# Kernel tuning notes

Hardware: AMD Instinct MI355X
Metric: run time of the kernel (lower is better)

Reference implementation:

```python
import jax, jax.numpy as jnp
import numpy as np

DIM = 512
HID = 2048
E = 16
B = 8
N = 2048
THRESHOLD = 0.8
CAP_FACTOR = 2.0  # eval mode
MIN_EXPERT_CAPACITY = 4
LOSS_COEF = 0.01
CAP = max(MIN_EXPERT_CAPACITY, min(N, int(N * CAP_FACTOR / E)))  # 256


def setup_inputs() -> dict:
    key = jax.random.key(0)
    k1, k2, k3, k4 = jax.random.split(key, 4)
    x = jax.random.normal(k1, (B, N, DIM), dtype=jnp.float32)
    w_gating = jax.random.normal(k2, (DIM, E), dtype=jnp.float32)
    std1 = 1.0 / np.sqrt(HID)
    std2 = 1.0 / np.sqrt(DIM)
    w1 = jax.random.uniform(k3, (E, DIM, HID), jnp.float32, -std1, std1)
    w2 = jax.random.uniform(k4, (E, HID, DIM), jnp.float32, -std2, std2)
    return {"x": x, "w_gating": w_gating, "w1": w1, "w2": w2}


def _gate(x, w_gating):
    # raw gate probabilities [B, N, E]
    raw = jax.nn.softmax(jnp.einsum('bnd,de->bne', x, w_gating), axis=-1)
    order = jnp.argsort(-raw, axis=-1)                      # descending sort indices
    sp = jnp.take_along_axis(raw, order, axis=-1)           # sorted probs (desc)
    cum = jnp.cumsum(sp, axis=-1)
    tm = cum >= THRESHOLD
    k = jnp.argmax(tm.astype(jnp.float32), axis=-1) + 1     # dynamic k per token
    k = jnp.where(jnp.any(tm, axis=-1), k, E)
    # select top-k in sorted order, renormalize
    rank = jnp.arange(E)
    sel = (rank < k[..., None]).astype(raw.dtype)           # [B,N,E] sorted order
    selp = sp * sel
    normp = selp / jnp.sum(selp, axis=-1, keepdims=True)
    # scatter back to expert order via inverse permutation
    inv = jnp.argsort(order, axis=-1)
    mask = jnp.take_along_axis(sel, inv, axis=-1)           # expert_masks [B,N,E]
    weights = jnp.take_along_axis(normp, inv, axis=-1)      # expert_weights
    # capacity: exclusive cumsum over tokens
    pos = (jnp.cumsum(mask, axis=-2) - mask) * mask
    mask = mask * (pos < float(CAP)).astype(mask.dtype)
    pos = pos * mask
    pos_tok = jnp.sum(pos, axis=-1).astype(jnp.int32)       # [B,N] (summed across experts, as in source)
    in_cap = (pos_tok < CAP).astype(raw.dtype)
    oh = jax.nn.one_hot(pos_tok, CAP, dtype=raw.dtype) * in_cap[..., None]  # [B,N,CAP]
    dispatch = mask[..., None] * oh[..., None, :]           # [B,N,E,CAP]
    combine = (weights * mask)[..., None] * oh[..., None, :]
    density = jnp.mean(mask, axis=-2)
    density_proxy = jnp.mean(raw, axis=-2)
    loss = jnp.mean(density_proxy * density) * float(E * E)
    loss = loss + 0.0 * jnp.mean(k.astype(jnp.float32))
    return dispatch, combine, loss


def reference(x, w_gating, w1, w2):
    dispatch, combine, loss = _gate(x, w_gating)
    expert_inputs = jnp.einsum('bnd,bnec->ebcd', x, dispatch)        # [E,B,CAP,D]
    ei = expert_inputs.reshape(E, B * CAP, DIM)
    hidden = jax.nn.gelu(jnp.einsum('end,edh->enh', ei, w1), approximate=False)
    eo = jnp.einsum('enh,ehd->end', hidden, w2).reshape(E, B, CAP, DIM)
    output = jnp.einsum('ebcd,bnec->bnd', eo, combine)               # [B,N,D]
    return output, loss * LOSS_COEF
```

## Files before the change

### kernel.cpp

```cpp
#include <hip/hip_runtime.h>
#include <math.h>

#define DIMC 512
#define HIDC 2048
#define EC   16
#define BC   8
#define NC   2048
#define CAPC 256
#define BN   (BC * NC)
#define THRESH 0.8f

typedef unsigned short u16;
typedef __attribute__((ext_vector_type(8))) __bf16 bf16x8;
typedef __attribute__((ext_vector_type(4))) float f32x4;

__device__ __forceinline__ float bf2f(unsigned u) {
    union { unsigned i; float f; } v; v.i = u << 16; return v.f;
}
__device__ __forceinline__ u16 f2bf(float f) {
    union { float f; unsigned i; } v; v.f = f;
    unsigned r = v.i + 0x7fff + ((v.i >> 16) & 1);
    return (u16)(r >> 16);
}
__device__ __forceinline__ float gelu_f(float x) {
    float u = 0.7978845608028654f * (x + 0.044715f * x * x * x);
    float t = __expf(2.f * u);
    float th = 1.f - 2.f / (t + 1.f);
    return 0.5f * x * (1.f + th);
}

__global__ void init_kernel(int* __restrict__ heads, int* __restrict__ pos_tok)
{
    int i = blockIdx.x * 256 + threadIdx.x;
    if (i < EC * BC * CAPC) heads[i] = -1;
    if (i < BN) pos_tok[i] = 0;
}

__global__ void wgt_kernel(const float* __restrict__ wg, float* __restrict__ wgt)
{
    int i = blockIdx.x * 256 + threadIdx.x;
    int e = i >> 9, d = i & 511;
    wgt[i] = wg[d * EC + e];
}

__global__ __launch_bounds__(256) void gate_kernel(const float* __restrict__ x,
                                                   const float* __restrict__ wgt,
                                                   float* __restrict__ raw,
                                                   float* __restrict__ weights,
                                                   float* __restrict__ maskf)
{
    __shared__ float lg[16][17];
    int t = threadIdx.x;
    int tok16 = t >> 4, e = t & 15;
    int token0 = blockIdx.x * 16;
    const float4* xr = (const float4*)(x + (size_t)(token0 + tok16) * DIMC);
    const float4* wr = (const float4*)(wgt + (size_t)e * DIMC);

    float a0 = 0.f, a1 = 0.f, a2 = 0.f, a3 = 0.f;
#pragma unroll 2
    for (int i = 0; i < 128; i += 4) {
        float4 xa = xr[i], xb = xr[i+1], xc = xr[i+2], xd = xr[i+3];
        float4 wa = wr[i], wb = wr[i+1], wc = wr[i+2], wd = wr[i+3];
        a0 = fmaf(xa.w, wa.w, fmaf(xa.z, wa.z, fmaf(xa.y, wa.y, fmaf(xa.x, wa.x, a0))));
        a1 = fmaf(xb.w, wb.w, fmaf(xb.z, wb.z, fmaf(xb.y, wb.y, fmaf(xb.x, wb.x, a1))));
        a2 = fmaf(xc.w, wc.w, fmaf(xc.z, wc.z, fmaf(xc.y, wc.y, fmaf(xc.x, wc.x, a2))));
        a3 = fmaf(xd.w, wd.w, fmaf(xd.z, wd.z, fmaf(xd.y, wd.y, fmaf(xd.x, wd.x, a3))));
    }
    lg[tok16][e] = (a0 + a1) + (a2 + a3);
    __syncthreads();
    if (t < 16) {
        int token = token0 + t;
        float p[EC];
#pragma unroll
        for (int j = 0; j < EC; ++j) p[j] = lg[t][j];

        float m = p[0];
#pragma unroll
        for (int j = 1; j < EC; ++j) m = fmaxf(m, p[j]);
        float s = 0.f;
#pragma unroll
        for (int j = 0; j < EC; ++j) { p[j] = expf(p[j] - m); s += p[j]; }
        float inv = 1.f / s;
#pragma unroll
        for (int j = 0; j < EC; ++j) p[j] *= inv;

        int rank[EC]; float cum[EC];
#pragma unroll
        for (int a = 0; a < EC; ++a) {
            int r = 0; float c = p[a];
#pragma unroll
            for (int j = 0; j < EC; ++j) {
                if (j == a) continue;
                bool ahead = (p[j] > p[a]) || (p[j] == p[a] && j < a);
                r += ahead ? 1 : 0;
                c += ahead ? p[j] : 0.f;
            }
            rank[a] = r; cum[a] = c;
        }
        int kr = EC - 1;
#pragma unroll
        for (int a = 0; a < EC; ++a)
            if (cum[a] >= THRESH) kr = min(kr, rank[a]);
        float denom = 0.f;
#pragma unroll
        for (int a = 0; a < EC; ++a) denom += (rank[a] <= kr) ? p[a] : 0.f;
        float invd = 1.f / denom;

        float w[EC], mk[EC];
#pragma unroll
        for (int a = 0; a < EC; ++a) {
            bool sel = rank[a] <= kr;
            w[a]  = sel ? p[a] * invd : 0.f;
            mk[a] = sel ? 1.f : 0.f;
        }
        float4* rp = (float4*)(raw + (size_t)token * EC);
        float4* wp = (float4*)(weights + (size_t)token * EC);
        float4* mp = (float4*)(maskf + (size_t)token * EC);
#pragma unroll
        for (int i = 0; i < 4; ++i) {
            rp[i] = make_float4(p[4*i], p[4*i+1], p[4*i+2], p[4*i+3]);
            wp[i] = make_float4(w[4*i], w[4*i+1], w[4*i+2], w[4*i+3]);
            mp[i] = make_float4(mk[4*i], mk[4*i+1], mk[4*i+2], mk[4*i+3]);
        }
    }
}

__global__ __launch_bounds__(64) void capacity_kernel(const float* __restrict__ raw,
                                                      float* __restrict__ maskf,
                                                      int* __restrict__ pos,
                                                      int* __restrict__ pos_tok,
                                                      float* __restrict__ density,
                                                      float* __restrict__ proxy)
{
    int t = blockIdx.x;
    int b = t / EC, e = t % EC;
    int lane = threadIdx.x;

    size_t idx = ((size_t)b * NC + lane) * EC + e;
    const size_t step = (size_t)64 * EC;
    float mv = maskf[idx];
    float rv = raw[idx];

    int count = 0;
    float rsum = 0.f;
    for (int n0 = 0; n0 < NC; n0 += 64) {
        float mn = 0.f, rn = 0.f;
        if (n0 + 64 < NC) { mn = maskf[idx + step]; rn = raw[idx + step]; }

        rsum += rv;
        unsigned long long bal = __ballot(mv != 0.f);
        int below = __popcll(bal & ((1ull << lane) - 1ull));
        int pval = 0;
        if (mv != 0.f) {
            pval = count + below;
            if (pval >= CAPC) { maskf[idx] = 0.f; pval = 0; }
            else if (pval > 0) atomicAdd(&pos_tok[b * NC + n0 + lane], pval);
        }
        pos[idx] = pval;
        count += __popcll(bal);

        idx += step; mv = mn; rv = rn;
    }
#pragma unroll
    for (int off = 32; off >= 1; off >>= 1) rsum += __shfl_xor(rsum, off);
    if (lane == 0) {
        int admitted = count < CAPC ? count : CAPC;
        density[t] = (float)admitted / (float)NC;
        proxy[t]   = rsum / (float)NC;
    }
}

__global__ __launch_bounds__(256) void build_kernel(const float* __restrict__ maskf,
                                                    const int* __restrict__ pos,
                                                    const int* __restrict__ pos_tok,
                                                    int* __restrict__ heads,
                                                    int* __restrict__ nxt,
                                                    int* __restrict__ node_tok)
{
    int id = blockIdx.x * 256 + threadIdx.x;
    int token = id >> 4, e = id & 15;
    if (maskf[id] == 0.f) return;
    int c = pos_tok[token];
    if (c >= CAPC) return;
    int b = token >> 11;
    int slot = (e * BC + b) * CAPC + c;
    int node = (e * BC + b) * CAPC + pos[id];
    node_tok[node] = token;
    nxt[node] = atomicExch(&heads[slot], node);
}

__global__ __launch_bounds__(256) void gather_ei_kernel(const float* __restrict__ x,
                                                        const int* __restrict__ heads,
                                                        const int* __restrict__ nxt,
                                                        const int* __restrict__ node_tok,
                                                        u16* __restrict__ ei)
{
    int slot = blockIdx.x * 4 + (threadIdx.x >> 6);
    int lane = threadIdx.x & 63;
    float a[8] = {0,0,0,0,0,0,0,0};
    int node = heads[slot];
    while (node >= 0) {
        const float4* xr = (const float4*)(x + (size_t)node_tok[node] * DIMC) + lane * 2;
        float4 v0 = xr[0], v1 = xr[1];
        a[0]+=v0.x; a[1]+=v0.y; a[2]+=v0.z; a[3]+=v0.w;
        a[4]+=v1.x; a[5]+=v1.y; a[6]+=v1.z; a[7]+=v1.w;
        node = nxt[node];
    }
    uint4 v;
    v.x = (unsigned)f2bf(a[0]) | ((unsigned)f2bf(a[1]) << 16);
    v.y = (unsigned)f2bf(a[2]) | ((unsigned)f2bf(a[3]) << 16);
    v.z = (unsigned)f2bf(a[4]) | ((unsigned)f2bf(a[5]) << 16);
    v.w = (unsigned)f2bf(a[6]) | ((unsigned)f2bf(a[7]) << 16);
    *(uint4*)(ei + (size_t)slot * DIMC + lane * 8) = v;
}

__global__ __launch_bounds__(256) void transpose_cvt_kernel(const float* __restrict__ in,
                                                            u16* __restrict__ out,
                                                            int R, int C)
{
    __shared__ float tile[64][65];
    size_t eoff = (size_t)blockIdx.z * R * C;
    int c0 = blockIdx.x * 64, r0 = blockIdx.y * 64;
    int tid = threadIdx.x;
    int rr = tid >> 4;
    int cc = (tid & 15) * 4;
#pragma unroll
    for (int i = 0; i < 4; ++i) {
        float4 v = *(const float4*)(in + eoff + (size_t)(r0 + rr + 16 * i) * C + c0 + cc);
        tile[rr + 16 * i][cc + 0] = v.x;
        tile[rr + 16 * i][cc + 1] = v.y;
        tile[rr + 16 * i][cc + 2] = v.z;
        tile[rr + 16 * i][cc + 3] = v.w;
    }
    __syncthreads();
    int c = tid >> 2;
    int r8 = (tid & 3) * 16;
    u16 buf[16];
#pragma unroll
    for (int j = 0; j < 16; ++j) buf[j] = f2bf(tile[r8 + j][c]);
    u16* op = out + eoff + (size_t)(c0 + c) * R + r0 + r8;
    *(uint4*)(op)     = *(uint4*)&buf[0];
    *(uint4*)(op + 8) = *(uint4*)&buf[8];
}

__device__ __forceinline__ void async_cp16(const u16* g, u16* l) {
    __builtin_amdgcn_global_load_lds(
        (const __attribute__((address_space(1))) unsigned*)g,
        (__attribute__((address_space(3))) unsigned*)l, 16, 0, 0);
}

template<int GELU>
__global__ __launch_bounds__(256) void gemm_bt_kernel(
    const u16* __restrict__ A, const u16* __restrict__ Bt, u16* __restrict__ C,
    int M, int N, int K, long sA, long sB, long sC)
{
    __shared__ __align__(16) u16 lds[2][2][128 * 64];
    int e = blockIdx.z;
    int bm = blockIdx.y * 128, bn = blockIdx.x * 128;
    int t = threadIdx.x, lane = t & 63, w = t >> 6;
    int wm = (w & 1) * 64, wn = (w >> 1) * 64;
    int q = lane >> 4, m16 = lane & 15;

    const u16* gA[4]; const u16* gB[4]; int lofs[4];
#pragma unroll
    for (int i = 0; i < 4; ++i) {
        int l = i * 256 + t, r = l >> 3, s = l & 7, c8 = s ^ (r & 7);
        gA[i] = A + (size_t)e * sA + (size_t)(bm + r) * K + c8 * 8;
        gB[i] = Bt + (size_t)e * sB + (size_t)(bn + r) * K + c8 * 8;
        lofs[i] = l * 8;
    }
    int aoff[4][2], boff[4][2];
#pragma unroll
    for (int i = 0; i < 4; ++i) {
        int ra = wm + i * 16 + m16, rb = wn + i * 16 + m16;
#pragma unroll
        for (int h = 0; h < 2; ++h) {
            int c8 = h * 4 + q;
            aoff[i][h] = (ra * 8 + (c8 ^ (ra & 7))) * 8;
            boff[i][h] = (rb * 8 + (c8 ^ (rb & 7))) * 8;
        }
    }

#pragma unroll
    for (int i = 0; i < 4; ++i) {
        async_cp16(gA[i], &lds[0][0][lofs[i]]);
        async_cp16(gB[i], &lds[0][1][lofs[i]]);
        gA[i] += 64; gB[i] += 64;
    }

    f32x4 acc[4][4] = {};
    int nk = K >> 6;
    for (int ki = 0; ki < nk; ++ki) {
        int cur = ki & 1, nx = cur ^ 1;
        __syncthreads();
        if (ki + 1 < nk) {
#pragma unroll
            for (int i = 0; i < 4; ++i) {
                async_cp16(gA[i], &lds[nx][0][lofs[i]]);
                async_cp16(gB[i], &lds[nx][1][lofs[i]]);
                gA[i] += 64; gB[i] += 64;
            }
        }
#pragma unroll
        for (int h = 0; h < 2; ++h) {
            bf16x8 af[4], bfr[4];
#pragma unroll
            for (int mt = 0; mt < 4; ++mt) af[mt] = *(const bf16x8*)&lds[cur][0][aoff[mt][h]];
#pragma unroll
            for (int nt = 0; nt < 4; ++nt) bfr[nt] = *(const bf16x8*)&lds[cur][1][boff[nt][h]];
#pragma unroll
            for (int mt = 0; mt < 4; ++mt)
#pragma unroll
                for (int nt = 0; nt < 4; ++nt)
                    acc[mt][nt] = __builtin_amdgcn_mfma_f32_16x16x32_bf16(
                        af[mt], bfr[nt], acc[mt][nt], 0, 0, 0);
        }
    }

    size_t cbase = (size_t)e * sC;
#pragma unroll
    for (int mt = 0; mt < 4; ++mt)
#pragma unroll
        for (int nt = 0; nt < 4; ++nt)
#pragma unroll
            for (int r2 = 0; r2 < 4; ++r2) {
                int row = bm + wm + mt * 16 + q * 4 + r2;
                int col = bn + wn + nt * 16 + m16;
                float v = acc[mt][nt][r2];
                if (GELU) v = gelu_f(v);
                C[cbase + (size_t)row * N + col] = f2bf(v);
            }
}

__global__ __launch_bounds__(256) void combine_kernel(const u16* __restrict__ eo,
                                                      const float* __restrict__ weights,
                                                      const float* __restrict__ maskf,
                                                      const int* __restrict__ pos_tok,
                                                      float* __restrict__ out)
{
    int token = blockIdx.x;
    int tid   = threadIdx.x;
    int b = token >> 11;
    int c = pos_tok[token];
    float a0 = 0.f, a1 = 0.f;
    if (c < CAPC) {
        const float* wr = weights + (size_t)token * EC;
        const float* mr = maskf   + (size_t)token * EC;
#pragma unroll
        for (int e = 0; e < EC; ++e) {
            float wm = wr[e] * mr[e];
            if (wm != 0.f) {
                const u16* src = eo + (((size_t)e * BC + b) * CAPC + c) * DIMC;
                unsigned u = *(const unsigned*)(src + 2 * tid);
                a0 += wm * bf2f(u & 0xffffu);
                a1 += wm * bf2f(u >> 16);
            }
        }
    }
    *(float2*)(out + (size_t)token * DIMC + 2 * tid) = make_float2(a0, a1);
}

__global__ void loss_kernel(const float* __restrict__ density,
                            const float* __restrict__ proxy,
                            float* __restrict__ out_loss)
{
    __shared__ float sh[BC * EC];
    int t = threadIdx.x;
    sh[t] = density[t] * proxy[t];
    __syncthreads();
    for (int s2 = (BC * EC) / 2; s2 >= 1; s2 >>= 1) {
        if (t < s2) sh[t] += sh[t + s2];
        __syncthreads();
    }
    if (t == 0)
        out_loss[0] = sh[0] * ((float)(EC * EC) / (float)(BC * EC)) * 0.01f;
}

extern "C" void kernel_launch(void* const* d_in, const int* in_sizes, int n_in,
                              void* d_out, int out_size, void* d_ws, size_t ws_size,
                              hipStream_t stream)
{
    const float* x  = (const float*)d_in[0];
    const float* wg = (const float*)d_in[1];
    const float* w1 = (const float*)d_in[2];
    const float* w2 = (const float*)d_in[3];
    float* out = (float*)d_out;

    char* ws = (char*)d_ws;
    size_t off = 0;
    auto alloc = [&](size_t bytes) -> void* {
        void* p = ws + off;
        off = (off + bytes + 255) & ~(size_t)255;
        return p;
    };
    float* raw      = (float*)alloc((size_t)BN * EC * 4);
    float* weights  = (float*)alloc((size_t)BN * EC * 4);
    float* maskf    = (float*)alloc((size_t)BN * EC * 4);
    int*   pos      = (int*)  alloc((size_t)BN * EC * 4);
    int*   pos_tok  = (int*)  alloc((size_t)BN * 4);
    int*   heads    = (int*)  alloc((size_t)EC * BC * CAPC * 4);
    int*   nxt      = (int*)  alloc((size_t)EC * BC * CAPC * 4);
    int*   node_tok = (int*)  alloc((size_t)EC * BC * CAPC * 4);
    float* density  = (float*)alloc(BC * EC * 4);
    float* proxy    = (float*)alloc(BC * EC * 4);
    float* wgt      = (float*)alloc((size_t)EC * DIMC * 4);
    u16*   ei_bf    = (u16*)alloc((size_t)EC * BC * CAPC * DIMC * 2);
    u16*   w1t      = (u16*)alloc((size_t)EC * DIMC * HIDC * 2);
    u16*   w2t      = (u16*)alloc((size_t)EC * HIDC * DIMC * 2);
    u16*   eo_bf    = (u16*)alloc((size_t)EC * BC * CAPC * DIMC * 2);
    size_t hid_full = (size_t)EC * BC * CAPC * HIDC * 2;
    int ngroups = (ws_size - off >= hid_full) ? 1 : 2;
    int EG = EC / ngroups;
    u16* hidden = (u16*)alloc((size_t)EG * BC * CAPC * HIDC * 2);

    (void)in_sizes; (void)n_in; (void)out_size;

    init_kernel<<<(EC * BC * CAPC + 255) / 256, 256, 0, stream>>>(heads, pos_tok);
    wgt_kernel<<<EC * DIMC / 256, 256, 0, stream>>>(wg, wgt);
    transpose_cvt_kernel<<<dim3(HIDC / 64, DIMC / 64, EC), 256, 0, stream>>>(w1, w1t, DIMC, HIDC);
    transpose_cvt_kernel<<<dim3(DIMC / 64, HIDC / 64, EC), 256, 0, stream>>>(w2, w2t, HIDC, DIMC);

    gate_kernel<<<BN / 16, 256, 0, stream>>>(x, wgt, raw, weights, maskf);
    capacity_kernel<<<BC * EC, 64, 0, stream>>>(raw, maskf, pos, pos_tok, density, proxy);
    build_kernel<<<BN * EC / 256, 256, 0, stream>>>(maskf, pos, pos_tok, heads, nxt, node_tok);
    gather_ei_kernel<<<EC * BC * CAPC / 4, 256, 0, stream>>>(x, heads, nxt, node_tok, ei_bf);

    for (int g = 0; g < ngroups; ++g) {
        const u16* Ag  = ei_bf + (size_t)g * EG * BC * CAPC * DIMC;
        const u16* B1g = w1t   + (size_t)g * EG * DIMC * HIDC;
        gemm_bt_kernel<1><<<dim3(HIDC / 128, (BC * CAPC) / 128, EG), 256, 0, stream>>>(
            Ag, B1g, hidden, BC * CAPC, HIDC, DIMC,
            (long)BC * CAPC * DIMC, (long)HIDC * DIMC, (long)BC * CAPC * HIDC);
        const u16* B2g = w2t + (size_t)g * EG * HIDC * DIMC;
        u16* Eg = eo_bf + (size_t)g * EG * BC * CAPC * DIMC;
        gemm_bt_kernel<0><<<dim3(DIMC / 128, (BC * CAPC) / 128, EG), 256, 0, stream>>>(
            hidden, B2g, Eg, BC * CAPC, DIMC, HIDC,
            (long)BC * CAPC * HIDC, (long)DIMC * HIDC, (long)BC * CAPC * DIMC);
    }

    combine_kernel<<<BN, 256, 0, stream>>>(eo_bf, weights, maskf, pos_tok, out);
    loss_kernel<<<1, BC * EC, 0, stream>>>(density, proxy, out + (size_t)BN * DIMC);
}
```

Measured before the change: 518.5 us.

## Fuse gating-weight transpose into gate kernel and parallelize routing via shuffles

Drops the separate wgt transpose kernel. Each gate block now loads the 512x16 gating matrix into LDS, transposing it on the way in, and reads weights from LDS instead of global memory. The softmax, ranking and top-k selection move from a single 16-thread serial section to wave shuffles across the 16 lanes of each token, so all 256 threads do routing work. The cost is a 33KB LDS tile reloaded in every block, which may limit occupancy and adds redundant global reads of the small weight matrix.

```diff
diff --git a/kernel.cpp b/kernel.cpp
--- a/kernel.cpp
+++ b/kernel.cpp
@@ -36,93 +36,83 @@
     if (i < BN) pos_tok[i] = 0;
 }
 
-__global__ void wgt_kernel(const float* __restrict__ wg, float* __restrict__ wgt)
-{
-    int i = blockIdx.x * 256 + threadIdx.x;
-    int e = i >> 9, d = i & 511;
-    wgt[i] = wg[d * EC + e];
-}
-
 __global__ __launch_bounds__(256) void gate_kernel(const float* __restrict__ x,
-                                                   const float* __restrict__ wgt,
+                                                   const float* __restrict__ wg,
                                                    float* __restrict__ raw,
                                                    float* __restrict__ weights,
                                                    float* __restrict__ maskf)
 {
-    __shared__ float lg[16][17];
+    __shared__ float wlds[16][516];
+    __shared__ float lg[16][16];
     int t = threadIdx.x;
     int tok16 = t >> 4, e = t & 15;
-    int token0 = blockIdx.x * 16;
-    const float4* xr = (const float4*)(x + (size_t)(token0 + tok16) * DIMC);
-    const float4* wr = (const float4*)(wgt + (size_t)e * DIMC);
-
+    int token = blockIdx.x * 16 + tok16;
+
+    {
+        const float4* wg4 = (const float4*)wg;
+#pragma unroll
+        for (int j = 0; j < 8; ++j) {
+            int idx4 = j * 256 + t;
+            float4 v = wg4[idx4];
+            int d  = idx4 >> 2;
+            int e0 = (idx4 & 3) * 4;
+            wlds[e0 + 0][d] = v.x;
+            wlds[e0 + 1][d] = v.y;
+            wlds[e0 + 2][d] = v.z;
+            wlds[e0 + 3][d] = v.w;
+        }
+    }
+    __syncthreads();
+
+    const float4* xr = (const float4*)(x + (size_t)token * DIMC);
+    const float4* wl = (const float4*)&wlds[e][0];
     float a0 = 0.f, a1 = 0.f, a2 = 0.f, a3 = 0.f;
-#pragma unroll 2
+#pragma unroll 4
     for (int i = 0; i < 128; i += 4) {
         float4 xa = xr[i], xb = xr[i+1], xc = xr[i+2], xd = xr[i+3];
-        float4 wa = wr[i], wb = wr[i+1], wc = wr[i+2], wd = wr[i+3];
+        float4 wa = wl[i], wb = wl[i+1], wc = wl[i+2], wd = wl[i+3];
         a0 = fmaf(xa.w, wa.w, fmaf(xa.z, wa.z, fmaf(xa.y, wa.y, fmaf(xa.x, wa.x, a0))));
         a1 = fmaf(xb.w, wb.w, fmaf(xb.z, wb.z, fmaf(xb.y, wb.y, fmaf(xb.x, wb.x, a1))));
         a2 = fmaf(xc.w, wc.w, fmaf(xc.z, wc.z, fmaf(xc.y, wc.y, fmaf(xc.x, wc.x, a2))));
         a3 = fmaf(xd.w, wd.w, fmaf(xd.z, wd.z, fmaf(xd.y, wd.y, fmaf(xd.x, wd.x, a3))));
     }
-    lg[tok16][e] = (a0 + a1) + (a2 + a3);
-    __syncthreads();
-    if (t < 16) {
-        int token = token0 + t;
-        float p[EC];
-#pragma unroll
-        for (int j = 0; j < EC; ++j) p[j] = lg[t][j];
-
-        float m = p[0];
-#pragma unroll
-        for (int j = 1; j < EC; ++j) m = fmaxf(m, p[j]);
-        float s = 0.f;
-#pragma unroll
-        for (int j = 0; j < EC; ++j) { p[j] = expf(p[j] - m); s += p[j]; }
-        float inv = 1.f / s;
-#pragma unroll
-        for (int j = 0; j < EC; ++j) p[j] *= inv;
-
-        int rank[EC]; float cum[EC];
-#pragma unroll
-        for (int a = 0; a < EC; ++a) {
-            int r = 0; float c = p[a];
-#pragma unroll
-            for (int j = 0; j < EC; ++j) {
-                if (j == a) continue;
-                bool ahead = (p[j] > p[a]) || (p[j] == p[a] && j < a);
-                r += ahead ? 1 : 0;
-                c += ahead ? p[j] : 0.f;
-            }
-            rank[a] = r; cum[a] = c;
-        }
-        int kr = EC - 1;
-#pragma unroll
-        for (int a = 0; a < EC; ++a)
-            if (cum[a] >= THRESH) kr = min(kr, rank[a]);
-        float denom = 0.f;
-#pragma unroll
-        for (int a = 0; a < EC; ++a) denom += (rank[a] <= kr) ? p[a] : 0.f;
-        float invd = 1.f / denom;
-
-        float w[EC], mk[EC];
-#pragma unroll
-        for (int a = 0; a < EC; ++a) {
-            bool sel = rank[a] <= kr;
-            w[a]  = sel ? p[a] * invd : 0.f;
-            mk[a] = sel ? 1.f : 0.f;
-        }
-        float4* rp = (float4*)(raw + (size_t)token * EC);
-        float4* wp = (float4*)(weights + (size_t)token * EC);
-        float4* mp = (float4*)(maskf + (size_t)token * EC);
-#pragma unroll
-        for (int i = 0; i < 4; ++i) {
-            rp[i] = make_float4(p[4*i], p[4*i+1], p[4*i+2], p[4*i+3]);
-            wp[i] = make_float4(w[4*i], w[4*i+1], w[4*i+2], w[4*i+3]);
-            mp[i] = make_float4(mk[4*i], mk[4*i+1], mk[4*i+2], mk[4*i+3]);
-        }
-    }
+    float logit = (a0 + a1) + (a2 + a3);
+
+    float m = logit;
+#pragma unroll
+    for (int off = 8; off >= 1; off >>= 1) m = fmaxf(m, __shfl_xor(m, off, 16));
+    float p = expf(logit - m);
+    float s = p;
+#pragma unroll
+    for (int off = 8; off >= 1; off >>= 1) s += __shfl_xor(s, off, 16);
+    p = p / s;
+
+    int rank = 0;
+    float cum = p;
+#pragma unroll
+    for (int j = 1; j < 16; ++j) {
+        float op = __shfl_xor(p, j, 16);
+        int oidx = e ^ j;
+        bool ahead = (op > p) || (op == p && oidx < e);
+        if (ahead) { rank++; cum += op; }
+    }
+    bool tm = (cum >= THRESH);
+    int kr = tm ? rank : (EC - 1);
+#pragma unroll
+    for (int off = 8; off >= 1; off >>= 1) kr = min(kr, __shfl_xor(kr, off, 16));
+    bool sel = (rank <= kr);
+
+    float dsel = sel ? p : 0.f;
+    float denom = dsel;
+#pragma unroll
+    for (int off = 8; off >= 1; off >>= 1) denom += __shfl_xor(denom, off, 16);
+    float w = sel ? (p / denom) : 0.f;
+
+    size_t o = (size_t)token * EC + e;
+    raw[o]     = p;
+    weights[o] = w;
+    maskf[o]   = sel ? 1.f : 0.f;
+    (void)lg;
 }
 
 __global__ __launch_bounds__(64) void capacity_kernel(const float* __restrict__ raw,
@@ -403,7 +393,6 @@
     int*   node_tok = (int*)  alloc((size_t)EC * BC * CAPC * 4);
     float* density  = (float*)alloc(BC * EC * 4);
     float* proxy    = (float*)alloc(BC * EC * 4);
-    float* wgt      = (float*)alloc((size_t)EC * DIMC * 4);
     u16*   ei_bf    = (u16*)alloc((size_t)EC * BC * CAPC * DIMC * 2);
     u16*   w1t      = (u16*)alloc((size_t)EC * DIMC * HIDC * 2);
     u16*   w2t      = (u16*)alloc((size_t)EC * HIDC * DIMC * 2);
@@ -416,11 +405,10 @@
     (void)in_sizes; (void)n_in; (void)out_size;
 
     init_kernel<<<(EC * BC * CAPC + 255) / 256, 256, 0, stream>>>(heads, pos_tok);
-    wgt_kernel<<<EC * DIMC / 256, 256, 0, stream>>>(wg, wgt);
     transpose_cvt_kernel<<<dim3(HIDC / 64, DIMC / 64, EC), 256, 0, stream>>>(w1, w1t, DIMC, HIDC);
     transpose_cvt_kernel<<<dim3(DIMC / 64, HIDC / 64, EC), 256, 0, stream>>>(w2, w2t, HIDC, DIMC);
 
-    gate_kernel<<<BN / 16, 256, 0, stream>>>(x, wgt, raw, weights, maskf);
+    gate_kernel<<<BN / 16, 256, 0, stream>>>(x, wg, raw, weights, maskf);
     capacity_kernel<<<BC * EC, 64, 0, stream>>>(raw, maskf, pos, pos_tok, density, proxy);
     build_kernel<<<BN * EC / 256, 256, 0, stream>>>(maskf, pos, pos_tok, heads, nxt, node_tok);
     gather_ei_kernel<<<EC * BC * CAPC / 4, 256, 0, stream>>>(x, heads, nxt, node_tok, ei_bf);
```

Result: faster. 470.1 us (-9.3%).
